# Performance work log

Hardware: AMD Instinct MI355X
Metric: run time of the kernel (lower is better)

## Reference

```python
import jax, jax.numpy as jnp
import numpy as np

BATCH, IN_DIM, HID, OUT_DIM, Z = 8192, 2048, 4096, 2048, 4
CONN_P = 0.5  # Bernoulli keep-probability y


def random_activation(h, ids):
    # ids: [dim] int32 in [0,5); per-channel nonlinearity applied over batch.
    ids = ids[None, :]
    return jnp.select(
        [ids == 0, ids == 1, ids == 2, ids == 3],
        [jax.nn.relu(h), jax.nn.sigmoid(h), jnp.tanh(h), jnp.where(h >= 0, h, 0.1 * h)],
        jax.nn.selu(h),
    )


def _make_linear(key, fan_in, fan_out):
    kw, kb, km = jax.random.split(key, 3)
    w = jax.random.normal(kw, (fan_out, fan_in), dtype=jnp.float32)
    mask = jax.random.bernoulli(km, CONN_P, (fan_out, fan_in)).astype(jnp.float32)
    b = jax.random.normal(kb, (fan_out,), dtype=jnp.float32)
    return w * mask, b


def setup_inputs() -> dict:
    key = jax.random.key(0)
    ks = jax.random.split(key, 16)
    inp = {"input_pattern": jax.random.normal(ks[0], (BATCH, IN_DIM), dtype=jnp.float32)}
    dims = [(IN_DIM, HID)] + [(HID, HID)] * Z + [(HID, OUT_DIM)]  # z+2 Linear layers
    for i, (fi, fo) in enumerate(dims):
        w, b = _make_linear(ks[1 + i], fi, fo)
        inp[f"w{i}"] = w
        inp[f"b{i}"] = b
        inp[f"ids{i}"] = jax.random.randint(ks[8 + i], (fo,), 0, 5, dtype=jnp.int32)
    return inp


def reference(input_pattern, w0, b0, ids0, w1, b1, ids1, w2, b2, ids2,
              w3, b3, ids3, w4, b4, ids4, w5, b5, ids5):
    ws = (w0, w1, w2, w3, w4, w5)
    bs = (b0, b1, b2, b3, b4, b5)
    ids = (ids0, ids1, ids2, ids3, ids4, ids5)
    h = input_pattern
    for w, b, i in zip(ws, bs, ids):
        h = random_activation(h @ w.T + b, i)
    return h
```

## Files before the change

kernel.cpp:

```cpp
#include <hip/hip_runtime.h>

typedef _Float16 f16;
typedef _Float16 f16x8 __attribute__((ext_vector_type(8)));
typedef float f32x4 __attribute__((ext_vector_type(4)));

#define BM 128
#define BN 128
#define BK 32

__device__ __forceinline__ void gload_lds16(const void* g, void* l) {
  __builtin_amdgcn_global_load_lds(
      (const __attribute__((address_space(1))) void*)g,
      (__attribute__((address_space(3))) void*)l,
      16, 0, 0);
}

__device__ __forceinline__ float act_apply(float x, int id) {
  switch (id) {
    case 0: return fmaxf(x, 0.0f);
    case 1: return 1.0f / (1.0f + __expf(-x));
    case 2: return tanhf(x);
    case 3: return x >= 0.0f ? x : 0.1f * x;
    default: return 1.0507009873554805f *
                    (x > 0.0f ? x : 1.6732632423543772f * expm1f(x));
  }
}

template <bool FINAL>
__global__ __launch_bounds__(256, 2)
void gemm_bias_act(const f16* __restrict__ A, const f16* __restrict__ W,
                   const float* __restrict__ bias, const int* __restrict__ ids,
                   float Sa, float invSn, void* __restrict__ outv,
                   int M, int N, int K) {
  __shared__ f16 lA[BM * BK];
  __shared__ f16 lB[BN * BK];

  const int tid  = (int)threadIdx.x;
  const int lane = tid & 63;
  const int wid  = tid >> 6;
  const int wr   = (wid >> 1) * 64;
  const int wc   = (wid & 1) * 64;

  const int nbx = N >> 7;
  const int nwg = (M >> 7) * nbx;
  const int b   = (int)blockIdx.x;
  const int swz = (b & 7) * (nwg >> 3) + (b >> 3);
  const int brow = (swz / nbx) << 7;
  const int bcol = (swz % nbx) << 7;

  const int srow = tid >> 2;
  const int scol = (tid & 3) << 3;
  const f16* gA0 = A + (long)(brow + srow) * K + scol;
  const f16* gA1 = gA0 + (long)64 * K;
  const f16* gB0 = W + (long)(bcol + srow) * K + scol;
  const f16* gB1 = gB0 + (long)64 * K;

  f16* ldA0 = &lA[tid * 8];
  f16* ldA1 = &lA[2048 + tid * 8];
  f16* ldB0 = &lB[tid * 8];
  f16* ldB1 = &lB[2048 + tid * 8];

  const int fr = lane & 15;
  const int k8 = (lane >> 4) << 3;

  f32x4 acc[4][4];
#pragma unroll
  for (int i = 0; i < 4; ++i)
#pragma unroll
    for (int j = 0; j < 4; ++j) acc[i][j] = (f32x4){0.f, 0.f, 0.f, 0.f};

  for (int kk = 0; kk < K; kk += BK) {
    gload_lds16(gA0 + kk, ldA0);
    gload_lds16(gA1 + kk, ldA1);
    gload_lds16(gB0 + kk, ldB0);
    gload_lds16(gB1 + kk, ldB1);
    __syncthreads();

    f16x8 af[4], bf[4];
#pragma unroll
    for (int m = 0; m < 4; ++m)
      af[m] = *(const f16x8*)&lA[(wr + m * 16 + fr) * BK + k8];
#pragma unroll
    for (int n = 0; n < 4; ++n)
      bf[n] = *(const f16x8*)&lB[(wc + n * 16 + fr) * BK + k8];

#pragma unroll
    for (int m = 0; m < 4; ++m)
#pragma unroll
      for (int n = 0; n < 4; ++n)
        acc[m][n] = __builtin_amdgcn_mfma_f32_16x16x32_f16(af[m], bf[n],
                                                           acc[m][n], 0, 0, 0);
    __syncthreads();
  }

  const int r4 = (lane >> 4) << 2;
#pragma unroll
  for (int n = 0; n < 4; ++n) {
    const int gcol = bcol + wc + n * 16 + fr;
    const float bv = bias[gcol];
    const int id   = ids[gcol];
#pragma unroll
    for (int m = 0; m < 4; ++m) {
      const int grow = brow + wr + m * 16 + r4;
#pragma unroll
      for (int i = 0; i < 4; ++i) {
        const float y = act_apply(acc[m][n][i] * Sa + bv, id);
        if (FINAL) {
          ((float*)outv)[(long)(grow + i) * N + gcol] = y;
        } else {
          ((f16*)outv)[(long)(grow + i) * N + gcol] = (f16)(y * invSn);
        }
      }
    }
  }
}

__global__ void cvt_f32_to_f16(const float* __restrict__ in, f16* __restrict__ out,
                               float scale, int n) {
  int i = ((int)blockIdx.x * 256 + (int)threadIdx.x) * 8;
  const int stride = (int)gridDim.x * 256 * 8;
  for (; i < n; i += stride) {
    const float4 v0 = *(const float4*)(in + i);
    const float4 v1 = *(const float4*)(in + i + 4);
    f16x8 h;
    h[0] = (f16)(v0.x * scale); h[1] = (f16)(v0.y * scale);
    h[2] = (f16)(v0.z * scale); h[3] = (f16)(v0.w * scale);
    h[4] = (f16)(v1.x * scale); h[5] = (f16)(v1.y * scale);
    h[6] = (f16)(v1.z * scale); h[7] = (f16)(v1.w * scale);
    *(f16x8*)(out + i) = h;
  }
}

extern "C" void kernel_launch(void* const* d_in, const int* in_sizes, int n_in,
                              void* d_out, int out_size, void* d_ws, size_t ws_size,
                              hipStream_t stream) {
  (void)in_sizes; (void)n_in; (void)out_size; (void)ws_size;
  const int M = 8192, IND = 2048, HID = 4096, OUTD = 2048;
  const float* x = (const float*)d_in[0];

  f16* actA = (f16*)d_ws;
  f16* actB = actA + (size_t)M * HID;
  f16* wbuf = actB + (size_t)M * HID;

  const float S[6] = {1.f, 16.f, 512.f, 16384.f, 262144.f, 8388608.f};

  const int Ks[6] = {IND, HID, HID, HID, HID, HID};
  const int Ns[6] = {HID, HID, HID, HID, HID, OUTD};

  cvt_f32_to_f16<<<2048, 256, 0, stream>>>(x, actA, 1.0f, M * IND);

  f16* cur = actA;
  f16* nxt = actB;
  for (int i = 0; i < 6; ++i) {
    const int K = Ks[i], N = Ns[i];
    const float* w  = (const float*)d_in[1 + 3 * i];
    const float* bs = (const float*)d_in[2 + 3 * i];
    const int* id   = (const int*)d_in[3 + 3 * i];

    cvt_f32_to_f16<<<2048, 256, 0, stream>>>(w, wbuf, 1.0f, N * K);

    const int nblk = (M >> 7) * (N >> 7);
    if (i < 5) {
      gemm_bias_act<false><<<nblk, 256, 0, stream>>>(
          cur, wbuf, bs, id, S[i], 1.0f / S[i + 1], nxt, M, N, K);
      f16* t = cur; cur = nxt; nxt = t;
    } else {
      gemm_bias_act<true><<<nblk, 256, 0, stream>>>(
          cur, wbuf, bs, id, S[i], 1.0f, d_out, M, N, K);
    }
  }
}
```

Measured before the change: 1.987 ms.

## Use 256x256 tiles with 4-stage LDS pipeline and XOR-swizzled shared layout

The GEMM moves from 128x128 tiles with 256 threads and a single LDS buffer to 256x256 tiles with 512 threads (8 waves, each computing 128x64). A 4-deep ring of LDS buffers is filled three stages ahead with direct global-to-LDS loads, paced by explicit vmcnt waits and raw barriers, so loads overlap the MFMA work. An XOR swizzle on the LDS layout is meant to remove bank conflicts on fragment reads, and s_setprio is raised around the MFMA block. The costs are 128KB of LDS per block, which likely limits occupancy to one block per CU, plus more accumulator registers per wave and only 512 blocks per layer on a 256-CU part.

```diff
diff --git a/kernel.cpp b/kernel.cpp
--- a/kernel.cpp
+++ b/kernel.cpp
@@ -4,15 +4,14 @@
 typedef _Float16 f16x8 __attribute__((ext_vector_type(8)));
 typedef float f32x4 __attribute__((ext_vector_type(4)));
 
-#define BM 128
-#define BN 128
+#define BM 256
+#define BN 256
 #define BK 32
 
 __device__ __forceinline__ void gload_lds16(const void* g, void* l) {
   __builtin_amdgcn_global_load_lds(
       (const __attribute__((address_space(1))) void*)g,
-      (__attribute__((address_space(3))) void*)l,
-      16, 0, 0);
+      (__attribute__((address_space(3))) void*)l, 16, 0, 0);
 }
 
 __device__ __forceinline__ float act_apply(float x, int id) {
@@ -27,81 +26,123 @@
 }
 
 template <bool FINAL>
-__global__ __launch_bounds__(256, 2)
+__global__ __launch_bounds__(512, 2)
 void gemm_bias_act(const f16* __restrict__ A, const f16* __restrict__ W,
                    const float* __restrict__ bias, const int* __restrict__ ids,
                    float Sa, float invSn, void* __restrict__ outv,
                    int M, int N, int K) {
-  __shared__ f16 lA[BM * BK];
-  __shared__ f16 lB[BN * BK];
+  __shared__ f16 lA[4][BM * BK];
+  __shared__ f16 lB[4][BN * BK];
 
   const int tid  = (int)threadIdx.x;
   const int lane = tid & 63;
   const int wid  = tid >> 6;
-  const int wr   = (wid >> 1) * 64;
-  const int wc   = (wid & 1) * 64;
-
-  const int nbx = N >> 7;
-  const int nwg = (M >> 7) * nbx;
+  const int wm   = wid >> 2;
+  const int wn   = wid & 3;
+
+  const int nbx = N >> 8;
+  const int nwg = (M >> 8) * nbx;
   const int b   = (int)blockIdx.x;
   const int swz = (b & 7) * (nwg >> 3) + (b >> 3);
-  const int brow = (swz / nbx) << 7;
-  const int bcol = (swz % nbx) << 7;
-
-  const int srow = tid >> 2;
-  const int scol = (tid & 3) << 3;
-  const f16* gA0 = A + (long)(brow + srow) * K + scol;
-  const f16* gA1 = gA0 + (long)64 * K;
-  const f16* gB0 = W + (long)(bcol + srow) * K + scol;
-  const f16* gB1 = gB0 + (long)64 * K;
-
-  f16* ldA0 = &lA[tid * 8];
-  f16* ldA1 = &lA[2048 + tid * 8];
-  f16* ldB0 = &lB[tid * 8];
-  f16* ldB1 = &lB[2048 + tid * 8];
+  const int brow = (swz / nbx) << 8;
+  const int bcol = (swz % nbx) << 8;
+
+  const int d0 = tid << 4;
+  const int d1 = d0 + 8192;
+  const int s0 = d0 ^ (((d0 >> 7) & 7) << 4);
+  const int s1 = d1 ^ (((d1 >> 7) & 7) << 4);
+  const int r0 = s0 >> 6, c0 = (s0 >> 4) & 3;
+  const int r1 = s1 >> 6, c1 = (s1 >> 4) & 3;
+
+  const f16* pA0 = A + (long)(brow + r0) * K + c0 * 8;
+  const f16* pA1 = A + (long)(brow + r1) * K + c1 * 8;
+  const f16* pB0 = W + (long)(bcol + r0) * K + c0 * 8;
+  const f16* pB1 = W + (long)(bcol + r1) * K + c1 * 8;
+  const int e0 = tid << 3;
+  const int e1 = e0 + 4096;
+
+#define STAGE(t)                                    \
+  do {                                              \
+    const int _s = (t) & 3;                         \
+    const long _k = (long)(t) << 5;                 \
+    gload_lds16(pA0 + _k, &lA[_s][e0]);             \
+    gload_lds16(pA1 + _k, &lA[_s][e1]);             \
+    gload_lds16(pB0 + _k, &lB[_s][e0]);             \
+    gload_lds16(pB1 + _k, &lB[_s][e1]);             \
+  } while (0)
 
   const int fr = lane & 15;
-  const int k8 = (lane >> 4) << 3;
-
-  f32x4 acc[4][4];
-#pragma unroll
-  for (int i = 0; i < 4; ++i)
-#pragma unroll
-    for (int j = 0; j < 4; ++j) acc[i][j] = (f32x4){0.f, 0.f, 0.f, 0.f};
-
-  for (int kk = 0; kk < K; kk += BK) {
-    gload_lds16(gA0 + kk, ldA0);
-    gload_lds16(gA1 + kk, ldA1);
-    gload_lds16(gB0 + kk, ldB0);
-    gload_lds16(gB1 + kk, ldB1);
-    __syncthreads();
-
-    f16x8 af[4], bf[4];
-#pragma unroll
-    for (int m = 0; m < 4; ++m)
-      af[m] = *(const f16x8*)&lA[(wr + m * 16 + fr) * BK + k8];
+  const int kb = lane >> 4;
+  const int xorv = ((fr >> 1) & 7) << 4;
+  const char* baA = (const char*)&lA[0][0];
+  const char* baB = (const char*)&lB[0][0];
+
+  int offA[8], offB[4];
+#pragma unroll
+  for (int m = 0; m < 8; ++m)
+    offA[m] = (((wm * 128 + m * 16 + fr) << 6) + (kb << 4)) ^ xorv;
+#pragma unroll
+  for (int n = 0; n < 4; ++n)
+    offB[n] = (((wn * 64 + n * 16 + fr) << 6) + (kb << 4)) ^ xorv;
+
+  f32x4 acc[8][4];
+#pragma unroll
+  for (int m = 0; m < 8; ++m)
+#pragma unroll
+    for (int n = 0; n < 4; ++n) acc[m][n] = (f32x4){0.f, 0.f, 0.f, 0.f};
+
+  const int nt = K >> 5;
+
+  STAGE(0);
+  STAGE(1);
+  STAGE(2);
+
+  for (int i = 0; i < nt; ++i) {
+    if (i + 3 < nt) {
+      STAGE(i + 3);
+      asm volatile("s_waitcnt vmcnt(12)" ::: "memory");
+    } else if (nt - 1 - i == 2) {
+      asm volatile("s_waitcnt vmcnt(8)" ::: "memory");
+    } else if (nt - 1 - i == 1) {
+      asm volatile("s_waitcnt vmcnt(4)" ::: "memory");
+    } else {
+      asm volatile("s_waitcnt vmcnt(0)" ::: "memory");
+    }
+    __builtin_amdgcn_s_barrier();
+    asm volatile("" ::: "memory");
+
+    const int so = (i & 3) << 14;
+    f16x8 af[8], bf[4];
+#pragma unroll
+    for (int m = 0; m < 8; ++m)
+      af[m] = *(const f16x8*)(baA + so + offA[m]);
 #pragma unroll
     for (int n = 0; n < 4; ++n)
-      bf[n] = *(const f16x8*)&lB[(wc + n * 16 + fr) * BK + k8];
-
-#pragma unroll
-    for (int m = 0; m < 4; ++m)
+      bf[n] = *(const f16x8*)(baB + so + offB[n]);
+
+    __builtin_amdgcn_s_setprio(1);
+#pragma unroll
+    for (int m = 0; m < 8; ++m)
 #pragma unroll
       for (int n = 0; n < 4; ++n)
         acc[m][n] = __builtin_amdgcn_mfma_f32_16x16x32_f16(af[m], bf[n],
                                                            acc[m][n], 0, 0, 0);
-    __syncthreads();
-  }
+    __builtin_amdgcn_s_setprio(0);
+
+    asm volatile("" ::: "memory");
+    __builtin_amdgcn_s_barrier();
+  }
+#undef STAGE
 
   const int r4 = (lane >> 4) << 2;
 #pragma unroll
   for (int n = 0; n < 4; ++n) {
-    const int gcol = bcol + wc + n * 16 + fr;
+    const int gcol = bcol + wn * 64 + n * 16 + fr;
     const float bv = bias[gcol];
     const int id   = ids[gcol];
 #pragma unroll
-    for (int m = 0; m < 4; ++m) {
-      const int grow = brow + wr + m * 16 + r4;
+    for (int m = 0; m < 8; ++m) {
+      const int grow = brow + wm * 128 + m * 16 + r4;
 #pragma unroll
       for (int i = 0; i < 4; ++i) {
         const float y = act_apply(acc[m][n][i] * Sa + bv, id);
@@ -159,13 +200,13 @@
 
     cvt_f32_to_f16<<<2048, 256, 0, stream>>>(w, wbuf, 1.0f, N * K);
 
-    const int nblk = (M >> 7) * (N >> 7);
+    const int nblk = (M >> 8) * (N >> 8);
     if (i < 5) {
-      gemm_bias_act<false><<<nblk, 256, 0, stream>>>(
+      gemm_bias_act<false><<<nblk, 512, 0, stream>>>(
           cur, wbuf, bs, id, S[i], 1.0f / S[i + 1], nxt, M, N, K);
       f16* t = cur; cur = nxt; nxt = t;
     } else {
-      gemm_bias_act<true><<<nblk, 256, 0, stream>>>(
+      gemm_bias_act<true><<<nblk, 512, 0, stream>>>(
           cur, wbuf, bs, id, S[i], 1.0f, d_out, M, N, K);
     }
   }
```

New measurement: 2.214 ms. 1.11x slower.

## Double-buffer GEMM LDS tiles with XOR swizzle and LDS-staged epilogue stores

Applied to the files above, without the earlier changes.

Rewrites the GEMM main loop to double-buffer the LDS tiles, so the next K-slice's global-to-LDS loads are issued before the MFMAs on the current slice, with one barrier per iteration instead of two. Adds an XOR swizzle to the LDS layout to cut bank conflicts on fragment reads. For intermediate layers the epilogue now stages results through LDS and writes 16-byte coalesced rows instead of scattered 2-byte stores. It also changes the block-to-tile mapping for L2 locality and raises launch-bounds occupancy hints (4, or 5 for layers 1 and 2), which may force register spills.

```diff
diff --git a/kernel.cpp b/kernel.cpp
--- a/kernel.cpp
+++ b/kernel.cpp
@@ -4,15 +4,10 @@
 typedef _Float16 f16x8 __attribute__((ext_vector_type(8)));
 typedef float f32x4 __attribute__((ext_vector_type(4)));
 
-#define BM 128
-#define BN 128
-#define BK 32
-
 __device__ __forceinline__ void gload_lds16(const void* g, void* l) {
   __builtin_amdgcn_global_load_lds(
       (const __attribute__((address_space(1))) void*)g,
-      (__attribute__((address_space(3))) void*)l,
-      16, 0, 0);
+      (__attribute__((address_space(3))) void*)l, 16, 0, 0);
 }
 
 __device__ __forceinline__ float act_apply(float x, int id) {
@@ -26,93 +21,158 @@
   }
 }
 
+#define GEMM128_BODY(FINAL)                                                   \
+  __shared__ f16 lA[2][128 * 32];                                             \
+  __shared__ f16 lB[2][128 * 32];                                             \
+                                                                              \
+  const int tid  = (int)threadIdx.x;                                          \
+  const int lane = tid & 63;                                                  \
+  const int wid  = tid >> 6;                                                  \
+  const int wr   = (wid >> 1) * 64;                                           \
+  const int wc   = (wid & 1) * 64;                                            \
+                                                                              \
+  const int nbc = N >> 7;                                                     \
+  const int b   = (int)blockIdx.x;                                            \
+  const int x   = b & 7;                                                      \
+  const int r   = b >> 3;                                                     \
+  int brow, bcol;                                                             \
+  if (nbc >= 32) {                                                            \
+    brow = ((x >> 1) * 16 + (r & 15)) << 7;                                   \
+    bcol = ((x & 1) * (nbc >> 1) + (r >> 4)) << 7;                            \
+  } else {                                                                    \
+    brow = (x * 8 + (r & 7)) << 7;                                            \
+    bcol = (r >> 3) << 7;                                                     \
+  }                                                                           \
+                                                                              \
+  const int d0 = tid << 4;                                                    \
+  const int d1 = d0 + 4096;                                                   \
+  const int s0 = d0 ^ (((d0 >> 7) & 7) << 4);                                 \
+  const int s1 = d1 ^ (((d1 >> 7) & 7) << 4);                                 \
+  const int r0 = s0 >> 6, c0 = (s0 >> 4) & 3;                                 \
+  const int r1 = s1 >> 6, c1 = (s1 >> 4) & 3;                                 \
+                                                                              \
+  const f16* pA0 = A + (long)(brow + r0) * K + c0 * 8;                        \
+  const f16* pA1 = A + (long)(brow + r1) * K + c1 * 8;                        \
+  const f16* pB0 = W + (long)(bcol + r0) * K + c0 * 8;                        \
+  const f16* pB1 = W + (long)(bcol + r1) * K + c1 * 8;                        \
+  const int e0 = tid << 3;                                                    \
+  const int e1 = e0 + 2048;                                                   \
+                                                                              \
+  const int fr = lane & 15;                                                   \
+  const int kb = lane >> 4;                                                   \
+  const int xorv = ((fr >> 1) & 7) << 4;                                      \
+                                                                              \
+  int offA[4], offB[4];                                                       \
+  _Pragma("unroll")                                                           \
+  for (int m = 0; m < 4; ++m)                                                 \
+    offA[m] = (((wr + m * 16 + fr) << 6) + (kb << 4)) ^ xorv;                 \
+  _Pragma("unroll")                                                           \
+  for (int n = 0; n < 4; ++n)                                                 \
+    offB[n] = (((wc + n * 16 + fr) << 6) + (kb << 4)) ^ xorv;                 \
+                                                                              \
+  f32x4 acc[4][4];                                                            \
+  _Pragma("unroll")                                                           \
+  for (int m = 0; m < 4; ++m)                                                 \
+    _Pragma("unroll")                                                         \
+    for (int n = 0; n < 4; ++n) acc[m][n] = (f32x4){0.f, 0.f, 0.f, 0.f};      \
+                                                                              \
+  const int nt = K >> 5;                                                      \
+  int buf = 0;                                                                \
+                                                                              \
+  gload_lds16(pA0, &lA[0][e0]);                                               \
+  gload_lds16(pA1, &lA[0][e1]);                                               \
+  gload_lds16(pB0, &lB[0][e0]);                                               \
+  gload_lds16(pB1, &lB[0][e1]);                                               \
+  __syncthreads();                                                            \
+                                                                              \
+  for (int t = 0; t < nt; ++t) {                                              \
+    if (t + 1 < nt) {                                                         \
+      const long kk = (long)(t + 1) << 5;                                     \
+      gload_lds16(pA0 + kk, &lA[buf ^ 1][e0]);                                \
+      gload_lds16(pA1 + kk, &lA[buf ^ 1][e1]);                                \
+      gload_lds16(pB0 + kk, &lB[buf ^ 1][e0]);                                \
+      gload_lds16(pB1 + kk, &lB[buf ^ 1][e1]);                                \
+    }                                                                         \
+    const char* bA = (const char*)&lA[buf][0];                                \
+    const char* bB = (const char*)&lB[buf][0];                                \
+    f16x8 af[4], bf[4];                                                       \
+    _Pragma("unroll")                                                         \
+    for (int m = 0; m < 4; ++m) af[m] = *(const f16x8*)(bA + offA[m]);        \
+    _Pragma("unroll")                                                         \
+    for (int n = 0; n < 4; ++n) bf[n] = *(const f16x8*)(bB + offB[n]);        \
+    _Pragma("unroll")                                                         \
+    for (int m = 0; m < 4; ++m)                                               \
+      _Pragma("unroll")                                                       \
+      for (int n = 0; n < 4; ++n)                                             \
+        acc[m][n] = __builtin_amdgcn_mfma_f32_16x16x32_f16(af[m], bf[n],      \
+                                                           acc[m][n], 0, 0, 0);\
+    if (t + 1 < nt) {                                                         \
+      __syncthreads();                                                        \
+      buf ^= 1;                                                               \
+    }                                                                         \
+  }                                                                           \
+                                                                              \
+  const int r4 = (lane >> 4) << 2;                                            \
+  if (!(FINAL)) {                                                             \
+    __syncthreads();                                                          \
+    char* eb = (char*)((wid < 2) ? &lA[wid][0] : &lB[wid - 2][0]);            \
+    _Pragma("unroll")                                                         \
+    for (int n = 0; n < 4; ++n) {                                             \
+      const int gcol = bcol + wc + n * 16 + fr;                               \
+      const float bv = bias[gcol];                                            \
+      const int id   = ids[gcol];                                             \
+      _Pragma("unroll")                                                       \
+      for (int m = 0; m < 4; ++m)                                             \
+        _Pragma("unroll")                                                     \
+        for (int i = 0; i < 4; ++i) {                                         \
+          const float y = act_apply(acc[m][n][i] * Sa + bv, id);              \
+          const int w = ((m * 16 + r4 + i) * 64 + n * 16 + fr) * 2;           \
+          *(f16*)(eb + (w ^ (((w >> 7) & 7) << 4))) = (f16)(y * invSn);       \
+        }                                                                     \
+    }                                                                         \
+    __syncthreads();                                                          \
+    f16* outp = (f16*)outv;                                                   \
+    _Pragma("unroll")                                                         \
+    for (int j = 0; j < 8; ++j) {                                             \
+      const int lrow = j * 8 + (lane >> 3);                                   \
+      const int rd = lrow * 128 + (lane & 7) * 16;                            \
+      const f16x8 v = *(const f16x8*)(eb + (rd ^ (((rd >> 7) & 7) << 4)));    \
+      *(f16x8*)&outp[(long)(brow + wr + lrow) * N + bcol + wc +               \
+                     (lane & 7) * 8] = v;                                     \
+    }                                                                         \
+  } else {                                                                    \
+    _Pragma("unroll")                                                         \
+    for (int n = 0; n < 4; ++n) {                                             \
+      const int gcol = bcol + wc + n * 16 + fr;                               \
+      const float bv = bias[gcol];                                            \
+      const int id   = ids[gcol];                                             \
+      _Pragma("unroll")                                                       \
+      for (int m = 0; m < 4; ++m) {                                           \
+        const int grow = brow + wr + m * 16 + r4;                             \
+        _Pragma("unroll")                                                     \
+        for (int i = 0; i < 4; ++i) {                                         \
+          const float y = act_apply(acc[m][n][i] * Sa + bv, id);              \
+          ((float*)outv)[(long)(grow + i) * N + gcol] = y;                    \
+        }                                                                     \
+      }                                                                       \
+    }                                                                         \
+  }
+
 template <bool FINAL>
-__global__ __launch_bounds__(256, 2)
-void gemm_bias_act(const f16* __restrict__ A, const f16* __restrict__ W,
-                   const float* __restrict__ bias, const int* __restrict__ ids,
-                   float Sa, float invSn, void* __restrict__ outv,
-                   int M, int N, int K) {
-  __shared__ f16 lA[BM * BK];
-  __shared__ f16 lB[BN * BK];
-
-  const int tid  = (int)threadIdx.x;
-  const int lane = tid & 63;
-  const int wid  = tid >> 6;
-  const int wr   = (wid >> 1) * 64;
-  const int wc   = (wid & 1) * 64;
-
-  const int nbx = N >> 7;
-  const int nwg = (M >> 7) * nbx;
-  const int b   = (int)blockIdx.x;
-  const int swz = (b & 7) * (nwg >> 3) + (b >> 3);
-  const int brow = (swz / nbx) << 7;
-  const int bcol = (swz % nbx) << 7;
-
-  const int srow = tid >> 2;
-  const int scol = (tid & 3) << 3;
-  const f16* gA0 = A + (long)(brow + srow) * K + scol;
-  const f16* gA1 = gA0 + (long)64 * K;
-  const f16* gB0 = W + (long)(bcol + srow) * K + scol;
-  const f16* gB1 = gB0 + (long)64 * K;
-
-  f16* ldA0 = &lA[tid * 8];
-  f16* ldA1 = &lA[2048 + tid * 8];
-  f16* ldB0 = &lB[tid * 8];
-  f16* ldB1 = &lB[2048 + tid * 8];
-
-  const int fr = lane & 15;
-  const int k8 = (lane >> 4) << 3;
-
-  f32x4 acc[4][4];
-#pragma unroll
-  for (int i = 0; i < 4; ++i)
-#pragma unroll
-    for (int j = 0; j < 4; ++j) acc[i][j] = (f32x4){0.f, 0.f, 0.f, 0.f};
-
-  for (int kk = 0; kk < K; kk += BK) {
-    gload_lds16(gA0 + kk, ldA0);
-    gload_lds16(gA1 + kk, ldA1);
-    gload_lds16(gB0 + kk, ldB0);
-    gload_lds16(gB1 + kk, ldB1);
-    __syncthreads();
-
-    f16x8 af[4], bf[4];
-#pragma unroll
-    for (int m = 0; m < 4; ++m)
-      af[m] = *(const f16x8*)&lA[(wr + m * 16 + fr) * BK + k8];
-#pragma unroll
-    for (int n = 0; n < 4; ++n)
-      bf[n] = *(const f16x8*)&lB[(wc + n * 16 + fr) * BK + k8];
-
-#pragma unroll
-    for (int m = 0; m < 4; ++m)
-#pragma unroll
-      for (int n = 0; n < 4; ++n)
-        acc[m][n] = __builtin_amdgcn_mfma_f32_16x16x32_f16(af[m], bf[n],
-                                                           acc[m][n], 0, 0, 0);
-    __syncthreads();
-  }
-
-  const int r4 = (lane >> 4) << 2;
-#pragma unroll
-  for (int n = 0; n < 4; ++n) {
-    const int gcol = bcol + wc + n * 16 + fr;
-    const float bv = bias[gcol];
-    const int id   = ids[gcol];
-#pragma unroll
-    for (int m = 0; m < 4; ++m) {
-      const int grow = brow + wr + m * 16 + r4;
-#pragma unroll
-      for (int i = 0; i < 4; ++i) {
-        const float y = act_apply(acc[m][n][i] * Sa + bv, id);
-        if (FINAL) {
-          ((float*)outv)[(long)(grow + i) * N + gcol] = y;
-        } else {
-          ((f16*)outv)[(long)(grow + i) * N + gcol] = (f16)(y * invSn);
-        }
-      }
-    }
-  }
+__global__ __launch_bounds__(256, 4)
+void gemm128(const f16* __restrict__ A, const f16* __restrict__ W,
+             const float* __restrict__ bias, const int* __restrict__ ids,
+             float Sa, float invSn, void* __restrict__ outv,
+             int M, int N, int K) {
+  GEMM128_BODY(FINAL)
+}
+
+__global__ __launch_bounds__(256, 5)
+void gemm128o(const f16* __restrict__ A, const f16* __restrict__ W,
+              const float* __restrict__ bias, const int* __restrict__ ids,
+              float Sa, float invSn, void* __restrict__ outv,
+              int M, int N, int K) {
+  GEMM128_BODY(false)
 }
 
 __global__ void cvt_f32_to_f16(const float* __restrict__ in, f16* __restrict__ out,
@@ -143,7 +203,6 @@
   f16* wbuf = actB + (size_t)M * HID;
 
   const float S[6] = {1.f, 16.f, 512.f, 16384.f, 262144.f, 8388608.f};
-
   const int Ks[6] = {IND, HID, HID, HID, HID, HID};
   const int Ns[6] = {HID, HID, HID, HID, HID, OUTD};
 
@@ -160,12 +219,16 @@
     cvt_f32_to_f16<<<2048, 256, 0, stream>>>(w, wbuf, 1.0f, N * K);
 
     const int nblk = (M >> 7) * (N >> 7);
-    if (i < 5) {
-      gemm_bias_act<false><<<nblk, 256, 0, stream>>>(
+    if (i == 1 || i == 2) {
+      gemm128o<<<nblk, 256, 0, stream>>>(
+          cur, wbuf, bs, id, S[i], 1.0f / S[i + 1], nxt, M, N, K);
+      f16* t = cur; cur = nxt; nxt = t;
+    } else if (i < 5) {
+      gemm128<false><<<nblk, 256, 0, stream>>>(
           cur, wbuf, bs, id, S[i], 1.0f / S[i + 1], nxt, M, N, K);
       f16* t = cur; cur = nxt; nxt = t;
     } else {
-      gemm_bias_act<true><<<nblk, 256, 0, stream>>>(
+      gemm128<true><<<nblk, 256, 0, stream>>>(
           cur, wbuf, bs, id, S[i], 1.0f, d_out, M, N, K);
     }
   }
```

Measured after the change: 3.711 ms. +86.8%, slower.
